# Performance work log

Measured on AMD Instinct MI355X. Metric: run time of the kernel, lower is better.

Reference implementation:

```python
import jax, jax.numpy as jnp
import numpy as np

N = 200000   # num_nodes
D = 64       # embedding_dims
B = 4096     # batch of target nodes (batched per-edge processing)
K = 128      # padded in-neighbor count per target
W = 20       # window_size (history deque length)
H = 128      # hidden_size


def setup_inputs() -> dict:
    key = jax.random.key(0)
    ks = jax.random.split(key, 14)
    return {
        "adj_time": jax.random.uniform(ks[0], (N,), jnp.float32),          # last-seen times in [0,1)
        "gc": jax.random.uniform(ks[1], (N,), jnp.float32),                 # per-node centrality scalar (dict_gc)
        "cur_time": jnp.ones((1,), jnp.float32),                            # current event time (>= all stored times)
        "neigh_mask": jnp.ones((B, K), jnp.float32),                        # 1 = valid neighbor slot
        "hist_feat": jax.random.normal(ks[2], (B, W, 2 * D), jnp.float32),  # feature_dict[...]['feature'] deque
        "hist_time": jax.random.uniform(ks[3], (B, W), jnp.float32),        # feature_dict[...]['time'] deque
        "t2v_w": jax.random.normal(ks[4], (D,), jnp.float32),               # Time2Vec('cos') weights
        "t2v_b": jax.random.normal(ks[5], (D,), jnp.float32),
        "node_w": jax.random.normal(ks[6], (D,), jnp.float32),              # linear_node: Linear(1, D)
        "node_b": jax.random.normal(ks[7], (D,), jnp.float32),
        "att_w": jax.random.normal(ks[8], (2 * D,), jnp.float32),           # Attention: score = cat(a,b) @ w + b
        "att_b": jax.random.normal(ks[9], (1,), jnp.float32),
        "weight": jax.random.normal(ks[10], (H, 4 * D), jnp.float32) * 0.05,
        "targets": jax.random.randint(ks[11], (B,), 0, N),
        "neigh_idx": jax.random.randint(ks[12], (B, K), 0, N),
    }


def reference(adj_time, gc, cur_time, neigh_mask, hist_feat, hist_time,
              t2v_w, t2v_b, node_w, node_b, att_w, att_b, weight,
              targets, neigh_idx):
    t = cur_time[0]

    def node_encoding(idx):
        # Time2Vec('cos'): first channel linear, rest cos(w*dt+b)
        dt = jnp.abs(t - adj_time[idx])[..., None]            # [..., 1]
        phase = t2v_w * dt + t2v_b                            # [..., D]
        tv = jnp.concatenate([phase[..., :1], jnp.cos(phase[..., 1:])], axis=-1)
        feat = jax.nn.relu(tv + gc[idx][..., None] * node_w + node_b)
        # F.normalize (L2 over feature dim)
        return feat / jnp.maximum(jnp.linalg.norm(feat, axis=-1, keepdims=True), 1e-12)

    tgt_feat = node_encoding(targets)       # [B, D]
    ngh_feat = node_encoding(neigh_idx)     # [B, K, D]

    # Decayer(2, 'log'): time_score = 1 / (2 * log(e + dt))
    time_score = 1.0 / (2.0 * jnp.log(jnp.e + (t - adj_time[neigh_idx])))   # [B, K]
    # Attention score between target and each neighbor encoding
    att = (tgt_feat @ att_w[:D])[:, None] \
        + jnp.einsum("bkd,d->bk", ngh_feat, att_w[D:]) + att_b[0]           # [B, K]
    score = jax.nn.leaky_relu(time_score + att, 0.01) * neigh_mask          # [B, K]
    neigh_agg = jnp.einsum("bk,bkd->bd", score, ngh_feat)                   # [B, D]

    combined = jnp.concatenate([tgt_feat, neigh_agg], axis=-1)              # [B, 2D]

    # History aggregation with Decayer(2, 'rev'): w = 1 / (2 * (1 + dt))
    hist_w = 1.0 / (2.0 * (1.0 + (t - hist_time)))                          # [B, W]
    hist_agg = jnp.einsum("bw,bwd->bd", hist_w, hist_feat)                  # [B, 2D]

    feat4 = jnp.concatenate([hist_agg, combined], axis=-1)                  # [B, 4D]
    return jax.nn.relu(feat4 @ weight.T)                                    # [B, H]
```

## Files before the change

### kernel.cpp

```cpp
#include <hip/hip_runtime.h>
#include <math.h>

#define NN 200000
#define DD 64
#define BB 4096
#define KK 128
#define WW 20
#define HH 128

__device__ __forceinline__ float fast_rcp(float x) { return __builtin_amdgcn_rcpf(x); }
__device__ __forceinline__ float fast_rsq(float x) { return __builtin_amdgcn_rsqf(x); }

__global__ __launch_bounds__(256) void k1_encode(
    const float* __restrict__ adj_time, const float* __restrict__ gc,
    const float* __restrict__ cur_time, const float* __restrict__ neigh_mask,
    const float* __restrict__ hist_feat, const float* __restrict__ hist_time,
    const float* __restrict__ t2v_w, const float* __restrict__ t2v_b,
    const float* __restrict__ node_w, const float* __restrict__ node_b,
    const float* __restrict__ att_w, const float* __restrict__ att_b,
    const int* __restrict__ targets, const int* __restrict__ neigh_idx,
    float* __restrict__ feat4)
{
    const int b    = blockIdx.x;
    const int tid  = threadIdx.x;
    const int lane = tid & 63;
    const int wid  = tid >> 6;
    const int k    = tid & 127;
    const int half = tid >> 7;

    __shared__ float  hws[WW];
    __shared__ float  hpart[128];
    __shared__ float4 dtg[128];
    __shared__ float2 sp[2][128];
    __shared__ float  aggp[4][64];
    __shared__ float  stL;

    const float t = cur_time[0];

    float ts_k = 0.f, m_k = 0.f;
    if (tid < 128) {
        int   idx = neigh_idx[b * KK + k];
        m_k       = neigh_mask[b * KK + k];
        float at  = adj_time[idx];
        float g   = gc[idx];
        float dt  = fabsf(t - at);
        dtg[k]    = make_float4(dt, g, 0.f, 0.f);
        ts_k      = fast_rcp(2.0f * __logf(2.71828182845904523536f + (t - at)));
    } else if (wid == 2) {
        if (lane < WW)
            hws[lane] = fast_rcp(2.0f * (1.0f + (t - hist_time[b * WW + lane])));
    } else {
        int   tg  = targets[b];
        float dtT = fabsf(t - adj_time[tg]);
        float gT  = gc[tg];
        float pw  = t2v_w[lane], pb = t2v_b[lane];
        float nw  = node_w[lane], nb2 = node_b[lane];
        float ph  = fmaf(pw, dtT, pb);
        float tv  = (lane == 0) ? ph : __cosf(ph);
        float f   = fmaxf(tv + fmaf(gT, nw, nb2), 0.f);
        float ss  = f * f;
#pragma unroll
        for (int off = 32; off; off >>= 1) ss += __shfl_xor(ss, off, 64);
        float invn = fast_rsq(fmaxf(ss, 1e-24f));
        float tfn  = f * invn;
        float sdt  = tfn * att_w[lane];
#pragma unroll
        for (int off = 32; off; off >>= 1) sdt += __shfl_xor(sdt, off, 64);
        if (lane == 0) stL = sdt;
        feat4[b * 256 + 128 + lane] = tfn;
    }
    __syncthreads();

    float hv[10];
    {
        const float* hf = hist_feat + (size_t)b * WW * 128 + (tid & 127);
#pragma unroll
        for (int w = 0; w < 10; ++w) hv[w] = hf[(half * 10 + w) * 128];
    }

    {
        const int du0 = __builtin_amdgcn_readfirstlane(half * 32);
        float4 dg = dtg[k];
        float  dt = dg.x, g = dg.y;
        float  s2 = 0.f, sd = 0.f;
#pragma unroll
        for (int dd = 0; dd < 32; ++dd) {
            int   d   = du0 + dd;
            float pw  = t2v_w[d], pb = t2v_b[d];
            float nw  = node_w[d], nb2 = node_b[d];
            float a2  = att_w[64 + d];
            float ph  = fmaf(pw, dt, pb);
            float cv  = __cosf(ph);
            float tv  = (d == 0) ? ph : cv;
            float f   = fmaxf(tv + fmaf(g, nw, nb2), 0.f);
            s2 = fmaf(f, f, s2);
            sd = fmaf(f, a2, sd);
        }
        sp[half][k] = make_float2(s2, sd);
    }

    float hsum = 0.f;
#pragma unroll
    for (int w = 0; w < 10; ++w) hsum = fmaf(hws[half * 10 + w], hv[w], hsum);
    if (half) hpart[tid & 127] = hsum;

    __syncthreads();

    if (!half) {
        feat4[b * 256 + (tid & 127)] = hsum + hpart[tid & 127];
        float2 a0 = sp[0][k], a1 = sp[1][k];
        float  s2 = a0.x + a1.x;
        float  sd = a0.y + a1.y;
        float  invn = fast_rsq(fmaxf(s2, 1e-24f));
        float  sc = ts_k + stL + sd * invn + att_b[0];
        sc = (sc > 0.f) ? sc : 0.01f * sc;
        dtg[k].z = sc * m_k * invn;
    }
    __syncthreads();

    {
        float pw  = t2v_w[lane], pb = t2v_b[lane];
        float nw  = node_w[lane], nb2 = node_b[lane];
        float acc = 0.f;
        const int k0 = wid * 32;
#pragma unroll 8
        for (int j = 0; j < 32; ++j) {
            float4 dg = dtg[k0 + j];
            float  ph = fmaf(pw, dg.x, pb);
            float  cv = __cosf(ph);
            float  tv = (lane == 0) ? ph : cv;
            float  f  = fmaxf(tv + fmaf(dg.y, nw, nb2), 0.f);
            acc = fmaf(dg.z, f, acc);
        }
        aggp[wid][lane] = acc;
    }
    __syncthreads();

    if (tid < 64) {
        feat4[b * 256 + 192 + tid] =
            aggp[0][tid] + aggp[1][tid] + aggp[2][tid] + aggp[3][tid];
    }
}

__global__ __launch_bounds__(256) void k2_gemm(
    const float* __restrict__ feat4, const float* __restrict__ weight,
    float* __restrict__ out)
{
    const int b0  = blockIdx.x * 8;
    const int tid = threadIdx.x;

    __shared__ float tile[8 * 256];
    __shared__ float wl[128 * 33];

    {
        const float4* src = (const float4*)(feat4 + (size_t)b0 * 256);
        float4* dst = (float4*)tile;
        dst[tid]       = src[tid];
        dst[tid + 256] = src[tid + 256];
    }

    const int h = tid & 127;
    const int g = tid >> 7;
    const float* tb = tile + (g * 4) * 256;

    float acc0 = 0.f, acc1 = 0.f, acc2 = 0.f, acc3 = 0.f;

    for (int c = 0; c < 8; ++c) {
        __syncthreads();
#pragma unroll
        for (int i = 0; i < 16; ++i) {
            int l  = i * 256 + tid;
            int hh = l >> 5;
            int jj = l & 31;
            wl[hh * 33 + jj] = weight[hh * 256 + c * 32 + jj];
        }
        __syncthreads();

#pragma unroll
        for (int jj = 0; jj < 32; jj += 4) {
            float w0 = wl[h * 33 + jj + 0];
            float w1 = wl[h * 33 + jj + 1];
            float w2 = wl[h * 33 + jj + 2];
            float w3 = wl[h * 33 + jj + 3];
            float4 f0 = *(const float4*)(tb + 0 * 256 + c * 32 + jj);
            float4 f1 = *(const float4*)(tb + 1 * 256 + c * 32 + jj);
            float4 f2 = *(const float4*)(tb + 2 * 256 + c * 32 + jj);
            float4 f3 = *(const float4*)(tb + 3 * 256 + c * 32 + jj);
            acc0 += w0 * f0.x + w1 * f0.y + w2 * f0.z + w3 * f0.w;
            acc1 += w0 * f1.x + w1 * f1.y + w2 * f1.z + w3 * f1.w;
            acc2 += w0 * f2.x + w1 * f2.y + w2 * f2.z + w3 * f2.w;
            acc3 += w0 * f3.x + w1 * f3.y + w2 * f3.z + w3 * f3.w;
        }
    }

    out[(size_t)(b0 + g * 4 + 0) * 128 + h] = fmaxf(acc0, 0.f);
    out[(size_t)(b0 + g * 4 + 1) * 128 + h] = fmaxf(acc1, 0.f);
    out[(size_t)(b0 + g * 4 + 2) * 128 + h] = fmaxf(acc2, 0.f);
    out[(size_t)(b0 + g * 4 + 3) * 128 + h] = fmaxf(acc3, 0.f);
}

extern "C" void kernel_launch(void* const* d_in, const int* in_sizes, int n_in,
                              void* d_out, int out_size, void* d_ws, size_t ws_size,
                              hipStream_t stream) {
    const float* adj_time  = (const float*)d_in[0];
    const float* gc        = (const float*)d_in[1];
    const float* cur_time  = (const float*)d_in[2];
    const float* neigh_mask= (const float*)d_in[3];
    const float* hist_feat = (const float*)d_in[4];
    const float* hist_time = (const float*)d_in[5];
    const float* t2v_w     = (const float*)d_in[6];
    const float* t2v_b     = (const float*)d_in[7];
    const float* node_w    = (const float*)d_in[8];
    const float* node_b    = (const float*)d_in[9];
    const float* att_w     = (const float*)d_in[10];
    const float* att_b     = (const float*)d_in[11];
    const float* weight    = (const float*)d_in[12];
    const int*   targets   = (const int*)d_in[13];
    const int*   neigh_idx = (const int*)d_in[14];

    float* out   = (float*)d_out;
    float* feat4 = (float*)d_ws;

    k1_encode<<<BB, 256, 0, stream>>>(adj_time, gc, cur_time, neigh_mask,
                                      hist_feat, hist_time, t2v_w, t2v_b,
                                      node_w, node_b, att_w, att_b,
                                      targets, neigh_idx, feat4);

    k2_gemm<<<BB / 8, 256, 0, stream>>>(feat4, weight, out);
}
```

Before: 137.0 us.

## Move history aggregation into GEMM kernel and cache encoder params in LDS

After: 146.4 us. 6.9% more time.

```diff
diff --git a/kernel.cpp b/kernel.cpp
--- a/kernel.cpp
+++ b/kernel.cpp
@@ -14,12 +14,11 @@
 __global__ __launch_bounds__(256) void k1_encode(
     const float* __restrict__ adj_time, const float* __restrict__ gc,
     const float* __restrict__ cur_time, const float* __restrict__ neigh_mask,
-    const float* __restrict__ hist_feat, const float* __restrict__ hist_time,
     const float* __restrict__ t2v_w, const float* __restrict__ t2v_b,
     const float* __restrict__ node_w, const float* __restrict__ node_b,
     const float* __restrict__ att_w, const float* __restrict__ att_b,
     const int* __restrict__ targets, const int* __restrict__ neigh_idx,
-    float* __restrict__ feat4)
+    float* __restrict__ feat2)
 {
     const int b    = blockIdx.x;
     const int tid  = threadIdx.x;
@@ -28,8 +27,8 @@
     const int k    = tid & 127;
     const int half = tid >> 7;
 
-    __shared__ float  hws[WW];
-    __shared__ float  hpart[128];
+    __shared__ float4 p4[64];
+    __shared__ float  aw2s[64];
     __shared__ float4 dtg[128];
     __shared__ float2 sp[2][128];
     __shared__ float  aggp[4][64];
@@ -43,21 +42,18 @@
         m_k       = neigh_mask[b * KK + k];
         float at  = adj_time[idx];
         float g   = gc[idx];
-        float dt  = fabsf(t - at);
-        dtg[k]    = make_float4(dt, g, 0.f, 0.f);
+        dtg[k]    = make_float4(fabsf(t - at), g, 0.f, 0.f);
         ts_k      = fast_rcp(2.0f * __logf(2.71828182845904523536f + (t - at)));
     } else if (wid == 2) {
-        if (lane < WW)
-            hws[lane] = fast_rcp(2.0f * (1.0f + (t - hist_time[b * WW + lane])));
+        p4[lane]   = make_float4(t2v_w[lane], t2v_b[lane], node_w[lane], node_b[lane]);
+        aw2s[lane] = att_w[64 + lane];
     } else {
         int   tg  = targets[b];
         float dtT = fabsf(t - adj_time[tg]);
         float gT  = gc[tg];
-        float pw  = t2v_w[lane], pb = t2v_b[lane];
-        float nw  = node_w[lane], nb2 = node_b[lane];
-        float ph  = fmaf(pw, dtT, pb);
+        float ph  = fmaf(t2v_w[lane], dtT, t2v_b[lane]);
         float tv  = (lane == 0) ? ph : __cosf(ph);
-        float f   = fmaxf(tv + fmaf(gT, nw, nb2), 0.f);
+        float f   = fmaxf(tv + fmaf(gT, node_w[lane], node_b[lane]), 0.f);
         float ss  = f * f;
 #pragma unroll
         for (int off = 32; off; off >>= 1) ss += __shfl_xor(ss, off, 64);
@@ -67,47 +63,32 @@
 #pragma unroll
         for (int off = 32; off; off >>= 1) sdt += __shfl_xor(sdt, off, 64);
         if (lane == 0) stL = sdt;
-        feat4[b * 256 + 128 + lane] = tfn;
-    }
-    __syncthreads();
-
-    float hv[10];
-    {
-        const float* hf = hist_feat + (size_t)b * WW * 128 + (tid & 127);
-#pragma unroll
-        for (int w = 0; w < 10; ++w) hv[w] = hf[(half * 10 + w) * 128];
-    }
-
-    {
-        const int du0 = __builtin_amdgcn_readfirstlane(half * 32);
+        feat2[b * 128 + lane] = tfn;
+    }
+    __syncthreads();
+
+    {
         float4 dg = dtg[k];
         float  dt = dg.x, g = dg.y;
         float  s2 = 0.f, sd = 0.f;
+        const int d0 = half * 32;
 #pragma unroll
         for (int dd = 0; dd < 32; ++dd) {
-            int   d   = du0 + dd;
-            float pw  = t2v_w[d], pb = t2v_b[d];
-            float nw  = node_w[d], nb2 = node_b[d];
-            float a2  = att_w[64 + d];
-            float ph  = fmaf(pw, dt, pb);
-            float cv  = __cosf(ph);
-            float tv  = (d == 0) ? ph : cv;
-            float f   = fmaxf(tv + fmaf(g, nw, nb2), 0.f);
+            int    d  = d0 + dd;
+            float4 p  = p4[d];
+            float  a2 = aw2s[d];
+            float  ph = fmaf(p.x, dt, p.y);
+            float  cv = __cosf(ph);
+            float  tv = (d == 0) ? ph : cv;
+            float  f  = fmaxf(tv + fmaf(g, p.z, p.w), 0.f);
             s2 = fmaf(f, f, s2);
             sd = fmaf(f, a2, sd);
         }
         sp[half][k] = make_float2(s2, sd);
     }
-
-    float hsum = 0.f;
-#pragma unroll
-    for (int w = 0; w < 10; ++w) hsum = fmaf(hws[half * 10 + w], hv[w], hsum);
-    if (half) hpart[tid & 127] = hsum;
-
     __syncthreads();
 
     if (!half) {
-        feat4[b * 256 + (tid & 127)] = hsum + hpart[tid & 127];
         float2 a0 = sp[0][k], a1 = sp[1][k];
         float  s2 = a0.x + a1.x;
         float  sd = a0.y + a1.y;
@@ -119,17 +100,16 @@
     __syncthreads();
 
     {
-        float pw  = t2v_w[lane], pb = t2v_b[lane];
-        float nw  = node_w[lane], nb2 = node_b[lane];
+        float4 pl = p4[lane];
         float acc = 0.f;
         const int k0 = wid * 32;
 #pragma unroll 8
         for (int j = 0; j < 32; ++j) {
             float4 dg = dtg[k0 + j];
-            float  ph = fmaf(pw, dg.x, pb);
+            float  ph = fmaf(pl.x, dg.x, pl.y);
             float  cv = __cosf(ph);
             float  tv = (lane == 0) ? ph : cv;
-            float  f  = fmaxf(tv + fmaf(dg.y, nw, nb2), 0.f);
+            float  f  = fmaxf(tv + fmaf(dg.y, pl.z, pl.w), 0.f);
             acc = fmaf(dg.z, f, acc);
         }
         aggp[wid][lane] = acc;
@@ -137,26 +117,52 @@
     __syncthreads();
 
     if (tid < 64) {
-        feat4[b * 256 + 192 + tid] =
+        feat2[b * 128 + 64 + tid] =
             aggp[0][tid] + aggp[1][tid] + aggp[2][tid] + aggp[3][tid];
     }
 }
 
 __global__ __launch_bounds__(256) void k2_gemm(
-    const float* __restrict__ feat4, const float* __restrict__ weight,
-    float* __restrict__ out)
+    const float* __restrict__ feat2, const float* __restrict__ weight,
+    const float* __restrict__ hist_feat, const float* __restrict__ hist_time,
+    const float* __restrict__ cur_time, float* __restrict__ out)
 {
     const int b0  = blockIdx.x * 8;
     const int tid = threadIdx.x;
 
     __shared__ float tile[8 * 256];
     __shared__ float wl[128 * 33];
-
-    {
-        const float4* src = (const float4*)(feat4 + (size_t)b0 * 256);
-        float4* dst = (float4*)tile;
-        dst[tid]       = src[tid];
-        dst[tid + 256] = src[tid + 256];
+    __shared__ float hwsL[8][WW];
+
+    const float t = cur_time[0];
+
+    if (tid < 8 * WW) {
+        int r = tid / WW, w = tid % WW;
+        hwsL[r][w] = fast_rcp(2.0f * (1.0f + (t - hist_time[(b0 + r) * WW + w])));
+    }
+    {
+        int fi = tid * 4;
+        int r  = fi >> 7;
+        int dc = fi & 127;
+        float4 v = *(const float4*)(feat2 + (size_t)(b0 + r) * 128 + dc);
+        *(float4*)(tile + r * 256 + 128 + dc) = v;
+    }
+    __syncthreads();
+
+    {
+        int d  = tid & 127;
+        int rg = tid >> 7;
+#pragma unroll
+        for (int rr = 0; rr < 4; ++rr) {
+            int r = rg * 4 + rr;
+            const float* hf = hist_feat + (size_t)(b0 + r) * WW * 128 + d;
+            float s = 0.f;
+#pragma unroll
+            for (int w = 0; w < WW; ++w) {
+                s = fmaf(hwsL[r][w], __builtin_nontemporal_load(hf + w * 128), s);
+            }
+            tile[r * 256 + d] = s;
+        }
     }
 
     const int h = tid & 127;
@@ -219,12 +225,12 @@
     const int*   neigh_idx = (const int*)d_in[14];
 
     float* out   = (float*)d_out;
-    float* feat4 = (float*)d_ws;
+    float* feat2 = (float*)d_ws;
 
     k1_encode<<<BB, 256, 0, stream>>>(adj_time, gc, cur_time, neigh_mask,
-                                      hist_feat, hist_time, t2v_w, t2v_b,
-                                      node_w, node_b, att_w, att_b,
-                                      targets, neigh_idx, feat4);
-
-    k2_gemm<<<BB / 8, 256, 0, stream>>>(feat4, weight, out);
+                                      t2v_w, t2v_b, node_w, node_b,
+                                      att_w, att_b, targets, neigh_idx, feat2);
+
+    k2_gemm<<<BB / 8, 256, 0, stream>>>(feat2, weight, hist_feat, hist_time,
+                                        cur_time, out);
 }
```
